# Performance work log

Measured on AMD Instinct MI355X. Metric: run time of the kernel, lower is better.

Reference implementation:

```python
import jax, jax.numpy as jnp
import numpy as np

# Static config (matches init_kwargs)
D_MODEL, H, L, P = 256, 8, 4, 4
HEAD_DIM = D_MODEL // H
SPATIAL = ((76, 114), (38, 57), (19, 29), (10, 15))  # (h, w) per level
NV = sum(h * w for h, w in SPATIAL)  # 11531
B, NQ = 2, NV


def setup_inputs() -> dict:
    key = jax.random.key(0)
    ks = jax.random.split(key, 12)
    inp = {
        "query": jax.random.normal(ks[0], (B, NQ, D_MODEL), jnp.float32),
        "reference_points": jax.random.uniform(ks[1], (B, NQ, L, 2), jnp.float32),
        "value": jax.random.normal(ks[2], (B, NV, D_MODEL), jnp.float32),
        # Linear params stored as [in, out] (i.e. torch weight transposed)
        "W_off": jax.random.normal(ks[3], (D_MODEL, H * L * P * 2), jnp.float32) * 0.02,
        "b_off": jax.random.normal(ks[4], (H * L * P * 2,), jnp.float32) * 0.5,
        "W_attn": jax.random.normal(ks[5], (D_MODEL, H * L * P), jnp.float32) * 0.02,
        "b_attn": jnp.zeros((H * L * P,), jnp.float32),
        "W_val": jax.random.normal(ks[6], (D_MODEL, D_MODEL), jnp.float32) * 0.05,
        "b_val": jnp.zeros((D_MODEL,), jnp.float32),
        "W_out": jax.random.normal(ks[7], (D_MODEL, D_MODEL), jnp.float32) * 0.05,
        "b_out": jnp.zeros((D_MODEL,), jnp.float32),
    }
    return inp


def _msda(query, reference_points, value, W_off, b_off, W_attn, b_attn,
          W_val, b_val, W_out, b_out):
    Bq, Nq, C = query.shape
    D = HEAD_DIM
    # value projection -> [B, H, Nv, D]
    v = (value @ W_val + b_val).reshape(Bq, -1, H, D).transpose(0, 2, 1, 3)
    # sampling locations: ref + offset / (w, h)  -> [B, Nq, H, L, P, 2] in [0,1] coords
    off = (query @ W_off + b_off).reshape(Bq, Nq, H, L, P, 2)
    wh = jnp.array([[w, h] for h, w in SPATIAL], dtype=query.dtype)  # [L, 2]
    loc = reference_points[:, :, None, :, None, :] + off / wh[None, None, None, :, None, :]
    # attention weights softmax over L*P  -> [B, H, Nq, L, P]
    attn = jax.nn.softmax((query @ W_attn + b_attn).reshape(Bq, Nq, H, L * P), axis=-1)
    attn = attn.reshape(Bq, Nq, H, L, P).transpose(0, 2, 1, 3, 4)
    starts = np.concatenate([[0], np.cumsum([h * w for h, w in SPATIAL])]).astype(int)
    out = jnp.zeros((Bq, H, Nq, D), query.dtype)
    for l, (lh, lw) in enumerate(SPATIAL):
        feat = v[:, :, starts[l]:starts[l + 1], :]  # [B, H, lh*lw, D]
        # grid_sample align_corners=False: pixel = loc * size - 0.5
        px = loc[:, :, :, l, :, 0].transpose(0, 2, 1, 3) * lw - 0.5  # [B, H, Nq, P]
        py = loc[:, :, :, l, :, 1].transpose(0, 2, 1, 3) * lh - 0.5
        x0 = jnp.floor(px)
        y0 = jnp.floor(py)
        samp = jnp.zeros(px.shape + (D,), query.dtype)
        for dx in (0, 1):
            for dy in (0, 1):
                xi = x0 + dx
                yi = y0 + dy
                w = (1.0 - jnp.abs(px - xi)) * (1.0 - jnp.abs(py - yi))
                valid = (xi >= 0) & (xi <= lw - 1) & (yi >= 0) & (yi <= lh - 1)
                idx = (jnp.clip(yi, 0, lh - 1) * lw + jnp.clip(xi, 0, lw - 1)).astype(jnp.int32)
                g = jnp.take_along_axis(feat, idx.reshape(Bq, H, -1)[..., None], axis=2)
                g = g.reshape(Bq, H, Nq, P, D)
                samp = samp + g * jnp.where(valid, w, 0.0)[..., None]
        out = out + jnp.einsum('bhnpd,bhnp->bhnd', samp, attn[:, :, :, l, :])
    out = out.transpose(0, 2, 1, 3).reshape(Bq, Nq, C)
    return out @ W_out + b_out


def reference(query, reference_points, value, W_off, b_off, W_attn, b_attn,
              W_val, b_val, W_out, b_out):
    return _msda(query, reference_points, value, W_off, b_off, W_attn, b_attn,
                 W_val, b_val, W_out, b_out)
```

## Files before the change

kernel.cpp:

```cpp
#include <hip/hip_runtime.h>
#include <cmath>

#define B_    2
#define NQ_   11531
#define NV_   11531
#define M_    (B_ * NQ_)
#define NCB_  2883

typedef unsigned short u16;
typedef unsigned int   u32;
typedef __attribute__((ext_vector_type(8))) short bf16x8;
typedef __attribute__((ext_vector_type(4))) float f32x4;

__device__ __forceinline__ u16 f2bf(float f) {
    union { float f; unsigned u; } v; v.f = f;
    unsigned r = v.u + 0x7FFFu + ((v.u >> 16) & 1u);
    return (u16)(r >> 16);
}
__device__ __forceinline__ float lo_bf(u32 u) {
    union { unsigned u; float f; } v; v.u = u << 16; return v.f;
}
__device__ __forceinline__ float hi_bf(u32 u) {
    union { unsigned u; float f; } v; v.u = u & 0xFFFF0000u; return v.f;
}

__device__ __forceinline__ int sort_key(const float* __restrict__ refp, int bq) {
    const int b = bq / NQ_;
    const float2 r = *(const float2*)&refp[(size_t)bq * 8];
    int qx = (int)(r.x * 32.f); qx = min(max(qx, 0), 31);
    int qy = (int)(r.y * 32.f); qy = min(max(qy, 0), 31);
    return b * 1024 + qy * 32 + qx;
}

__global__ __launch_bounds__(256) void transpose_hist_cast(
    const float* __restrict__ Wv, const float* __restrict__ Wo,
    const float* __restrict__ Wa, const float* __restrict__ Wu,
    const float* __restrict__ refp,
    const float* __restrict__ query, const float* __restrict__ value,
    u16* __restrict__ Tv, u16* __restrict__ Toa, u16* __restrict__ Tu,
    int* __restrict__ hist, u16* __restrict__ qbf, u16* __restrict__ vbf) {
    const int bid = blockIdx.x;
    const int tid = threadIdx.x;
    if (bid >= 347) {
        const int t8 = bid - 347;
        const bool isq = t8 < NCB_;
        const int cb = isq ? t8 : t8 - NCB_;
        const float* S = isq ? query : value;
        u16* D = isq ? qbf : vbf;
        const size_t TOT = (size_t)M_ * 256;
        const size_t e = ((size_t)cb * 256 + tid) * 8;
        if (e + 8 <= TOT) {
            const float4 a = *(const float4*)&S[e];
            const float4 b = *(const float4*)&S[e + 4];
            ushort4 lo, hi;
            lo.x = f2bf(a.x); lo.y = f2bf(a.y); lo.z = f2bf(a.z); lo.w = f2bf(a.w);
            hi.x = f2bf(b.x); hi.y = f2bf(b.y); hi.z = f2bf(b.z); hi.w = f2bf(b.w);
            *(ushort4*)&D[e] = lo;
            *(ushort4*)&D[e + 4] = hi;
        } else {
            for (size_t i = e; i < TOT; ++i) D[i] = f2bf(S[i]);
        }
        return;
    }
    if (bid >= 256) {
        const int bq = (bid - 256) * 256 + tid;
        if (bq < M_) atomicAdd(&hist[sort_key(refp, bq)], 1);
        return;
    }
    const int z = bid >> 6;
    const float* W; u16* T; int N; int rowoff = 0;
    if (z == 0)      { W = Wv; T = Tv;  N = 256; }
    else if (z == 1) { W = Wo; T = Toa; N = 256; }
    else if (z == 2) { W = Wa; T = Toa; N = 128; rowoff = 256; }
    else             { W = Wu; T = Tu;  N = 256; }
    const int rest = bid & 63;
    const int n0 = (rest & 7) * 32, k0 = (rest >> 3) * 32;
    if (n0 >= N) return;
    __shared__ float t[32][33];
    const int c = tid & 31, r0 = tid >> 5;
#pragma unroll
    for (int i = 0; i < 4; ++i)
        t[r0 + i * 8][c] = W[(size_t)(k0 + r0 + i * 8) * N + n0 + c];
    __syncthreads();
#pragma unroll
    for (int i = 0; i < 4; ++i)
        T[(size_t)(rowoff + n0 + r0 + i * 8) * 256 + k0 + c] = f2bf(t[c][r0 + i * 8]);
}

__device__ void scan_block(const int* __restrict__ hist, int* __restrict__ ofs,
                           int* part) {
    const int tid = threadIdx.x;
    const int base = tid * 8;
    int loc[8]; int s = 0;
#pragma unroll
    for (int i = 0; i < 8; ++i) { loc[i] = s; s += hist[base + i]; }
    part[tid] = s;
    __syncthreads();
    for (int d = 1; d < 256; d <<= 1) {
        const int v = part[tid];
        const int u = (tid >= d) ? part[tid - d] : 0;
        __syncthreads();
        part[tid] = v + u;
        __syncthreads();
    }
    const int off = (tid > 0) ? part[tid - 1] : 0;
#pragma unroll
    for (int i = 0; i < 8; ++i) ofs[base + i] = off + loc[i];
}

__global__ __launch_bounds__(256) void repack_scatter(
    const u16* __restrict__ ws_v, const float* __restrict__ refp,
    int* __restrict__ ofs, int* __restrict__ perm,
    u32* __restrict__ v3, int nsc) {
    const int bid = blockIdx.x;
    const int tid = threadIdx.x;
    if (bid < nsc) {
        const int bq = bid * 256 + tid;
        if (bq < M_) {
            const int pos = atomicAdd(&ofs[sort_key(refp, bq)], 1);
            perm[pos] = bq;
        }
        return;
    }
    const int g4 = (bid - nsc) * 256 + tid;
    if (g4 >= 8 * M_ * 8) return;
    const int h = g4 / (M_ * 8);
    const int rem = g4 - h * (M_ * 8);
    const int r = rem >> 3;
    const int c = (rem & 7) * 4;
    const ushort4 lo = *(const ushort4*)&ws_v[(size_t)r * 256 + h * 32 + c];
    ushort4 hi = make_ushort4(0, 0, 0, 0);
    if (r + 1 < M_) hi = *(const ushort4*)&ws_v[(size_t)(r + 1) * 256 + h * 32 + c];
    uint4 o;
    o.x = (u32)lo.x | ((u32)hi.x << 16);
    o.y = (u32)lo.y | ((u32)hi.y << 16);
    o.z = (u32)lo.z | ((u32)hi.z << 16);
    o.w = (u32)lo.w | ((u32)hi.w << 16);
    *(uint4*)&v3[((size_t)h * M_ + r) * 32 + c] = o;
}

template <int TN, int EPI>
__device__ __forceinline__ void gemm_body(const u16* __restrict__ A,
                                          const u16* __restrict__ WT,
                                          const float* __restrict__ bias,
                                          const float* __restrict__ bias2,
                                          void* __restrict__ Cv, int M,
                                          int bm, int bn,
                                          short* A_l, short* B_l) {
    constexpr int K = 256;
    const int tid = threadIdx.x;
    const int w = tid >> 6;
    const int lane = tid & 63;
    const int wr = (w >> 1) * 64;
    const int wc = (w & 1) * 64;
    const int lr = lane & 15;

    f32x4 acc[4][4] = {};

    for (int k0 = 0; k0 < K; k0 += 64) {
#pragma unroll
        for (int i = 0; i < 4; ++i) {
            const int vid = tid + i * 256;
            const int ar = vid >> 3;
            const int ak = (vid & 7) * 8;
            const int gr = bm + ar;
            uint4 hv = make_uint4(0u, 0u, 0u, 0u);
            if (gr < M) hv = *(const uint4*)&A[(size_t)gr * K + k0 + ak];
            *(uint4*)&A_l[ar * 72 + ak] = hv;
        }
#pragma unroll
        for (int i = 0; i < 4; ++i) {
            const int vid = tid + i * 256;
            const int nr = vid >> 3;
            const int kk = (vid & 7) * 8;
            const uint4 wv = *(const uint4*)&WT[(size_t)(bn + nr) * K + k0 + kk];
            *(uint4*)&B_l[nr * 72 + kk] = wv;
        }
        __syncthreads();
#pragma unroll
        for (int half = 0; half < 2; ++half) {
            const int kg = half * 32 + (lane >> 4) * 8;
            bf16x8 af[4], bfr[4];
#pragma unroll
            for (int m = 0; m < 4; ++m)
                af[m] = *(const bf16x8*)&A_l[(wr + m * 16 + lr) * 72 + kg];
#pragma unroll
            for (int n = 0; n < 4; ++n)
                bfr[n] = *(const bf16x8*)&B_l[(wc + n * 16 + lr) * 72 + kg];
#pragma unroll
            for (int m = 0; m < 4; ++m)
#pragma unroll
                for (int n = 0; n < 4; ++n)
                    acc[m][n] = __builtin_amdgcn_mfma_f32_16x16x32_bf16(af[m], bfr[n], acc[m][n], 0, 0, 0);
        }
        __syncthreads();
    }

#pragma unroll
    for (int n = 0; n < 4; ++n) {
        const int gcol = bn + wc + n * 16 + lr;
        const float bv = (TN == 384 && gcol >= 256) ? bias2[gcol - 256] : bias[gcol];
#pragma unroll
        for (int m = 0; m < 4; ++m) {
            const int rbase = bm + wr + m * 16 + (lane >> 4) * 4;
#pragma unroll
            for (int j = 0; j < 4; ++j) {
                const int grow = rbase + j;
                if (grow < M) {
                    const float o = acc[m][n][j] + bv;
                    if constexpr (EPI == 1) ((u16*)Cv)[(size_t)grow * TN + gcol] = f2bf(o);
                    else                    ((float*)Cv)[(size_t)grow * TN + gcol] = o;
                }
            }
        }
    }
}

__global__ __launch_bounds__(256, 4) void gemm_stage1(
    const u16* __restrict__ qbf, const u16* __restrict__ vbf,
    const u16* __restrict__ WT_val, const u16* __restrict__ WT_oa,
    const float* __restrict__ b_val, const float* __restrict__ b_off,
    const float* __restrict__ b_attn,
    const int* __restrict__ hist, int* __restrict__ ofs,
    u16* __restrict__ ws_v, float* __restrict__ ws_oa, int M, int gy) {
    __shared__ __align__(16) short A_l[128 * 72];
    __shared__ __align__(16) short B_l[128 * 72];
    int blk = blockIdx.x;
    if (blk == 5 * gy) {
        scan_block(hist, ofs, (int*)A_l);
    } else if (blk < 2 * gy) {
        gemm_body<256, 1>(vbf, WT_val, b_val, b_val, ws_v, M,
                          (blk >> 1) * 128, (blk & 1) * 128, A_l, B_l);
    } else {
        blk -= 2 * gy;
        gemm_body<384, 0>(qbf, WT_oa, b_off, b_attn, ws_oa, M,
                          (blk / 3) * 128, (blk % 3) * 128, A_l, B_l);
    }
}

__global__ __launch_bounds__(256, 4) void gemm_out(
    const u16* __restrict__ samp, const u16* __restrict__ WT_out,
    const float* __restrict__ b_out, float* __restrict__ out, int M) {
    __shared__ __align__(16) short A_l[128 * 72];
    __shared__ __align__(16) short B_l[128 * 72];
    const int blk = blockIdx.x;
    gemm_body<256, 0>(samp, WT_out, b_out, b_out, out, M,
                      (blk >> 1) * 128, (blk & 1) * 128, A_l, B_l);
}

__global__ __launch_bounds__(512, 4) void msda_sample_v10(
    const u32* __restrict__ v3,
    const float* __restrict__ oa,
    const float* __restrict__ refp,
    const int* __restrict__ perm,
    u16* __restrict__ samp) {
    __shared__ __align__(16) float4 s_w4[1088];
    __shared__ __align__(8)  int2   s_i2[1088];
    __shared__ int s_bq[8];
    const int tid = threadIdx.x;

    const int nwg = gridDim.x;
    const int qq = nwg >> 3, rr = nwg & 7;
    const int xcd = blockIdx.x & 7, pos = blockIdx.x >> 3;
    const int wg = (xcd < rr ? xcd * (qq + 1) : rr * (qq + 1) + (xcd - rr) * qq) + pos;
    const int bq0 = wg * 8;

    if (tid < 8) {
        const int q = bq0 + tid;
        s_bq[tid] = perm[q < M_ ? q : M_ - 1];
    }
    __syncthreads();

#pragma unroll
    for (int half = 0; half < 2; ++half) {
        const int s = tid + half * 512;
        const int qi = s >> 7;
        const int rem = s & 127;
        const int sampi = rem & 15;
        const int l = sampi >> 2;
        const int h = rem >> 4;
        const int bq = s_bq[qi];
        const int b = bq / NQ_;

        const float logit = oa[(size_t)bq * 384 + 256 + rem];
        float mx = logit;
#pragma unroll
        for (int t = 8; t >= 1; t >>= 1) mx = fmaxf(mx, __shfl_xor(mx, t, 16));
        const float e = __expf(logit - mx);
        float sm = e;
#pragma unroll
        for (int t = 8; t >= 1; t >>= 1) sm += __shfl_xor(sm, t, 16);
        const float aw = e / sm;

        const float2 off = *(const float2*)&oa[(size_t)bq * 384 + rem * 2];
        const float2 rxy = *(const float2*)&refp[(size_t)bq * 8 + l * 2];
        const int lw = (l == 0) ? 114 : (l == 1) ? 57 : (l == 2) ? 29 : 15;
        const int lh = (l == 0) ? 76 : (l == 1) ? 38 : (l == 2) ? 19 : 10;
        const int st = (l == 0) ? 0 : (l == 1) ? 8664 : (l == 2) ? 10830 : 11381;
        const int base = b * NV_ + st;

        const float px = rxy.x * (float)lw + off.x - 0.5f;
        const float py = rxy.y * (float)lh + off.y - 0.5f;
        const float x0f = floorf(px), y0f = floorf(py);
        const int x0 = (int)x0f, y0 = (int)y0f;
        const float fx = px - x0f, fy = py - y0f;

        float wxlo = 0.f, wxhi = 0.f;
        if (x0 >= 0 && x0 < lw)      wxlo = 1.f - fx;
        else if (x0 == -1)           wxlo = fx;
        if (x0 >= 0 && x0 + 1 < lw)  wxhi = fx;
        const int xs = min(max(x0, 0), lw - 1);

        const float wy0 = (y0 >= 0 && y0 < lh) ? (1.f - fy) : 0.f;
        const float wy1 = (y0 + 1 >= 0 && y0 + 1 < lh) ? fy : 0.f;
        const int ys0 = min(max(y0, 0), lh - 1);
        const int ys1 = min(max(y0 + 1, 0), lh - 1);

        const int hrow = h * M_;
        int2 iv;
        iv.x = (hrow + base + ys0 * lw + xs) << 7;
        iv.y = (hrow + base + ys1 * lw + xs) << 7;
        float4 wv;
        wv.x = aw * wxlo * wy0; wv.y = aw * wxhi * wy0;
        wv.z = aw * wxlo * wy1; wv.w = aw * wxhi * wy1;
        const int slot = (qi * 8 + h) * 17 + sampi;
        s_w4[slot] = wv;
        s_i2[slot] = iv;
    }
    __syncthreads();

    const int qi = tid >> 6;
    const int lane = tid & 63;
    const int h = lane >> 3;
    const int lcoff = (lane & 7) * 16;
    const int bq = s_bq[qi];
    const int sb = (qi * 8 + h) * 17;
    const char* vb = (const char*)v3;

    float acc0 = 0.f, acc1 = 0.f, acc2 = 0.f, acc3 = 0.f;
    float4 wc = s_w4[sb];
    int2 ic = s_i2[sb];
    uint4 A0 = *(const uint4*)(vb + (u32)(ic.x + lcoff));
    uint4 A1 = *(const uint4*)(vb + (u32)(ic.y + lcoff));

#pragma unroll 2
    for (int sp = 0; sp < 16; ++sp) {
        const int nxt = (sp + 1) & 15;
        const float4 wn = s_w4[sb + nxt];
        const int2 in_ = s_i2[sb + nxt];
        const uint4 B0 = *(const uint4*)(vb + (u32)(in_.x + lcoff));
        const uint4 B1 = *(const uint4*)(vb + (u32)(in_.y + lcoff));

        acc0 = fmaf(wc.x, lo_bf(A0.x), acc0); acc0 = fmaf(wc.y, hi_bf(A0.x), acc0);
        acc0 = fmaf(wc.z, lo_bf(A1.x), acc0); acc0 = fmaf(wc.w, hi_bf(A1.x), acc0);
        acc1 = fmaf(wc.x, lo_bf(A0.y), acc1); acc1 = fmaf(wc.y, hi_bf(A0.y), acc1);
        acc1 = fmaf(wc.z, lo_bf(A1.y), acc1); acc1 = fmaf(wc.w, hi_bf(A1.y), acc1);
        acc2 = fmaf(wc.x, lo_bf(A0.z), acc2); acc2 = fmaf(wc.y, hi_bf(A0.z), acc2);
        acc2 = fmaf(wc.z, lo_bf(A1.z), acc2); acc2 = fmaf(wc.w, hi_bf(A1.z), acc2);
        acc3 = fmaf(wc.x, lo_bf(A0.w), acc3); acc3 = fmaf(wc.y, hi_bf(A0.w), acc3);
        acc3 = fmaf(wc.z, lo_bf(A1.w), acc3); acc3 = fmaf(wc.w, hi_bf(A1.w), acc3);

        wc = wn; A0 = B0; A1 = B1;
    }
    if (bq0 + qi < M_) {
        ushort4 o;
        o.x = f2bf(acc0); o.y = f2bf(acc1); o.z = f2bf(acc2); o.w = f2bf(acc3);
        *(ushort4*)&samp[(size_t)bq * 256 + (h * 32 + (lane & 7) * 4)] = o;
    }
}

extern "C" void kernel_launch(void* const* d_in, const int* in_sizes, int n_in,
                              void* d_out, int out_size, void* d_ws, size_t ws_size,
                              hipStream_t stream) {
    const float* query  = (const float*)d_in[0];
    const float* refp   = (const float*)d_in[1];
    const float* value  = (const float*)d_in[2];
    const float* W_off  = (const float*)d_in[3];
    const float* b_off  = (const float*)d_in[4];
    const float* W_attn = (const float*)d_in[5];
    const float* b_attn = (const float*)d_in[6];
    const float* W_val  = (const float*)d_in[7];
    const float* b_val  = (const float*)d_in[8];
    const float* W_out  = (const float*)d_in[9];
    const float* b_out  = (const float*)d_in[10];
    float* out = (float*)d_out;

    const int M = M_;
    u16*   ws_v    = (u16*)d_ws;
    u16*   ws_samp = ws_v;
    u32*   ws_v3   = (u32*)(ws_v + (size_t)M * 256);
    u16*   vbf     = (u16*)ws_v3;
    float* ws_oa   = (float*)(ws_v3 + (size_t)8 * M * 32);
    u16*   qbf     = (u16*)(ws_oa + (size_t)M * 384);
    u16*   WT_val  = qbf + (size_t)M * 256;
    u16*   WT_oa   = WT_val + 256 * 256;
    u16*   WT_out  = WT_oa + 384 * 256;
    int*   hist    = (int*)(WT_out + 256 * 256);
    int*   ofs     = hist + 2048;
    int*   perm    = ofs + 2048;

    const int gy = (M + 127) / 128;
    const int gq = (M + 255) / 256;
    const int grep = (8 * M * 8 + 255) / 256;

    hipMemsetAsync(hist, 0, 2048 * sizeof(int), stream);
    transpose_hist_cast<<<dim3(347 + 2 * NCB_), 256, 0, stream>>>(
        W_val, W_off, W_attn, W_out, refp, query, value,
        WT_val, WT_oa, WT_out, hist, qbf, vbf);
    gemm_stage1<<<dim3(5 * gy + 1), 256, 0, stream>>>(qbf, vbf, WT_val, WT_oa,
                                                      b_val, b_off, b_attn,
                                                      hist, ofs, ws_v, ws_oa, M, gy);
    repack_scatter<<<dim3(gq + grep), 256, 0, stream>>>(ws_v, refp, ofs, perm,
                                                        ws_v3, gq);
    msda_sample_v10<<<dim3((M + 7) / 8), 512, 0, stream>>>(ws_v3, ws_oa, refp, perm, ws_samp);
    gemm_out<<<dim3(2 * gy), 256, 0, stream>>>(ws_samp, WT_out, b_out, out, M);
}
```

Measured before the change: 113.7 us.

## Shrink GEMM tiles to 64x64 with K=32 steps and pack sampling FMAs

The shared GEMM body moves from 128x128 tiles with K steps of 64 to 64x64 tiles with K steps of 32. This quadruples the number of blocks and raises the occupancy hint to 8, so more workgroups cover the ~23k-row problems with less LDS per block. In exchange each tile does less reuse and hits more barriers per K. Separately, the sampling kernel's bilinear accumulation uses two-wide float vectors so the compiler can emit packed FMA (v_pk_fma), with the two partial sums added at the end. That changes the floating-point summation order slightly.

```diff
diff --git a/kernel.cpp b/kernel.cpp
--- a/kernel.cpp
+++ b/kernel.cpp
@@ -11,17 +11,17 @@
 typedef unsigned int   u32;
 typedef __attribute__((ext_vector_type(8))) short bf16x8;
 typedef __attribute__((ext_vector_type(4))) float f32x4;
+typedef __attribute__((ext_vector_type(2))) float f32x2;
 
 __device__ __forceinline__ u16 f2bf(float f) {
     union { float f; unsigned u; } v; v.f = f;
     unsigned r = v.u + 0x7FFFu + ((v.u >> 16) & 1u);
     return (u16)(r >> 16);
 }
-__device__ __forceinline__ float lo_bf(u32 u) {
-    union { unsigned u; float f; } v; v.u = u << 16; return v.f;
-}
-__device__ __forceinline__ float hi_bf(u32 u) {
-    union { unsigned u; float f; } v; v.u = u & 0xFFFF0000u; return v.f;
+__device__ __forceinline__ f32x2 unpk(u32 u) {
+    union { unsigned u; float f; } lo, hi;
+    lo.u = u << 16; hi.u = u & 0xFFFF0000u;
+    f32x2 r; r.x = lo.f; r.y = hi.f; return r;
 }
 
 __device__ __forceinline__ int sort_key(const float* __restrict__ refp, int bq) {
@@ -151,57 +151,50 @@
     const int tid = threadIdx.x;
     const int w = tid >> 6;
     const int lane = tid & 63;
-    const int wr = (w >> 1) * 64;
-    const int wc = (w & 1) * 64;
+    const int wr = (w >> 1) * 32;
+    const int wc = (w & 1) * 32;
     const int lr = lane & 15;
-
-    f32x4 acc[4][4] = {};
-
-    for (int k0 = 0; k0 < K; k0 += 64) {
-#pragma unroll
-        for (int i = 0; i < 4; ++i) {
-            const int vid = tid + i * 256;
-            const int ar = vid >> 3;
-            const int ak = (vid & 7) * 8;
+    const int kg = (lane >> 4) * 8;
+
+    f32x4 acc[2][2] = {};
+
+    for (int k0 = 0; k0 < K; k0 += 32) {
+        {
+            const int ar = tid >> 2;
+            const int ak = (tid & 3) * 8;
             const int gr = bm + ar;
             uint4 hv = make_uint4(0u, 0u, 0u, 0u);
             if (gr < M) hv = *(const uint4*)&A[(size_t)gr * K + k0 + ak];
-            *(uint4*)&A_l[ar * 72 + ak] = hv;
+            *(uint4*)&A_l[ar * 40 + ak] = hv;
         }
-#pragma unroll
-        for (int i = 0; i < 4; ++i) {
-            const int vid = tid + i * 256;
-            const int nr = vid >> 3;
-            const int kk = (vid & 7) * 8;
+        {
+            const int nr = tid >> 2;
+            const int kk = (tid & 3) * 8;
             const uint4 wv = *(const uint4*)&WT[(size_t)(bn + nr) * K + k0 + kk];
-            *(uint4*)&B_l[nr * 72 + kk] = wv;
+            *(uint4*)&B_l[nr * 40 + kk] = wv;
         }
         __syncthreads();
-#pragma unroll
-        for (int half = 0; half < 2; ++half) {
-            const int kg = half * 32 + (lane >> 4) * 8;
-            bf16x8 af[4], bfr[4];
-#pragma unroll
-            for (int m = 0; m < 4; ++m)
-                af[m] = *(const bf16x8*)&A_l[(wr + m * 16 + lr) * 72 + kg];
-#pragma unroll
-            for (int n = 0; n < 4; ++n)
-                bfr[n] = *(const bf16x8*)&B_l[(wc + n * 16 + lr) * 72 + kg];
-#pragma unroll
-            for (int m = 0; m < 4; ++m)
-#pragma unroll
-                for (int n = 0; n < 4; ++n)
-                    acc[m][n] = __builtin_amdgcn_mfma_f32_16x16x32_bf16(af[m], bfr[n], acc[m][n], 0, 0, 0);
-        }
+        bf16x8 af[2], bfr[2];
+#pragma unroll
+        for (int m = 0; m < 2; ++m)
+            af[m] = *(const bf16x8*)&A_l[(wr + m * 16 + lr) * 40 + kg];
+#pragma unroll
+        for (int n = 0; n < 2; ++n)
+            bfr[n] = *(const bf16x8*)&B_l[(wc + n * 16 + lr) * 40 + kg];
+#pragma unroll
+        for (int m = 0; m < 2; ++m)
+#pragma unroll
+            for (int n = 0; n < 2; ++n)
+                acc[m][n] = __builtin_amdgcn_mfma_f32_16x16x32_bf16(af[m], bfr[n], acc[m][n], 0, 0, 0);
         __syncthreads();
     }
 
 #pragma unroll
-    for (int n = 0; n < 4; ++n) {
+    for (int n = 0; n < 2; ++n) {
         const int gcol = bn + wc + n * 16 + lr;
         const float bv = (TN == 384 && gcol >= 256) ? bias2[gcol - 256] : bias[gcol];
 #pragma unroll
-        for (int m = 0; m < 4; ++m) {
+        for (int m = 0; m < 2; ++m) {
             const int rbase = bm + wr + m * 16 + (lane >> 4) * 4;
 #pragma unroll
             for (int j = 0; j < 4; ++j) {
@@ -216,39 +209,40 @@
     }
 }
 
-__global__ __launch_bounds__(256, 4) void gemm_stage1(
+__global__ __launch_bounds__(256, 8) void gemm_stage1(
     const u16* __restrict__ qbf, const u16* __restrict__ vbf,
     const u16* __restrict__ WT_val, const u16* __restrict__ WT_oa,
     const float* __restrict__ b_val, const float* __restrict__ b_off,
     const float* __restrict__ b_attn,
     const int* __restrict__ hist, int* __restrict__ ofs,
-    u16* __restrict__ ws_v, float* __restrict__ ws_oa, int M, int gy) {
-    __shared__ __align__(16) short A_l[128 * 72];
-    __shared__ __align__(16) short B_l[128 * 72];
+    u16* __restrict__ ws_v, float* __restrict__ ws_oa, int M, int gy64) {
+    __shared__ __align__(16) short A_l[64 * 40];
+    __shared__ __align__(16) short B_l[64 * 40];
+    __shared__ int part[256];
     int blk = blockIdx.x;
-    if (blk == 5 * gy) {
-        scan_block(hist, ofs, (int*)A_l);
-    } else if (blk < 2 * gy) {
+    if (blk == 10 * gy64) {
+        scan_block(hist, ofs, part);
+    } else if (blk < 4 * gy64) {
         gemm_body<256, 1>(vbf, WT_val, b_val, b_val, ws_v, M,
-                          (blk >> 1) * 128, (blk & 1) * 128, A_l, B_l);
+                          (blk >> 2) * 64, (blk & 3) * 64, A_l, B_l);
     } else {
-        blk -= 2 * gy;
+        blk -= 4 * gy64;
         gemm_body<384, 0>(qbf, WT_oa, b_off, b_attn, ws_oa, M,
-                          (blk / 3) * 128, (blk % 3) * 128, A_l, B_l);
-    }
-}
-
-__global__ __launch_bounds__(256, 4) void gemm_out(
+                          (blk / 6) * 64, (blk % 6) * 64, A_l, B_l);
+    }
+}
+
+__global__ __launch_bounds__(256, 8) void gemm_out(
     const u16* __restrict__ samp, const u16* __restrict__ WT_out,
     const float* __restrict__ b_out, float* __restrict__ out, int M) {
-    __shared__ __align__(16) short A_l[128 * 72];
-    __shared__ __align__(16) short B_l[128 * 72];
+    __shared__ __align__(16) short A_l[64 * 40];
+    __shared__ __align__(16) short B_l[64 * 40];
     const int blk = blockIdx.x;
     gemm_body<256, 0>(samp, WT_out, b_out, b_out, out, M,
-                      (blk >> 1) * 128, (blk & 1) * 128, A_l, B_l);
-}
-
-__global__ __launch_bounds__(512, 4) void msda_sample_v10(
+                      (blk >> 2) * 64, (blk & 3) * 64, A_l, B_l);
+}
+
+__global__ __launch_bounds__(512, 4) void msda_sample_v11(
     const u32* __restrict__ v3,
     const float* __restrict__ oa,
     const float* __restrict__ refp,
@@ -337,8 +331,8 @@
     const int sb = (qi * 8 + h) * 17;
     const char* vb = (const char*)v3;
 
-    float acc0 = 0.f, acc1 = 0.f, acc2 = 0.f, acc3 = 0.f;
-    float4 wc = s_w4[sb];
+    f32x2 acc0 = {0.f, 0.f}, acc1 = {0.f, 0.f}, acc2 = {0.f, 0.f}, acc3 = {0.f, 0.f};
+    float4 wcur = s_w4[sb];
     int2 ic = s_i2[sb];
     uint4 A0 = *(const uint4*)(vb + (u32)(ic.x + lcoff));
     uint4 A1 = *(const uint4*)(vb + (u32)(ic.y + lcoff));
@@ -351,20 +345,19 @@
         const uint4 B0 = *(const uint4*)(vb + (u32)(in_.x + lcoff));
         const uint4 B1 = *(const uint4*)(vb + (u32)(in_.y + lcoff));
 
-        acc0 = fmaf(wc.x, lo_bf(A0.x), acc0); acc0 = fmaf(wc.y, hi_bf(A0.x), acc0);
-        acc0 = fmaf(wc.z, lo_bf(A1.x), acc0); acc0 = fmaf(wc.w, hi_bf(A1.x), acc0);
-        acc1 = fmaf(wc.x, lo_bf(A0.y), acc1); acc1 = fmaf(wc.y, hi_bf(A0.y), acc1);
-        acc1 = fmaf(wc.z, lo_bf(A1.y), acc1); acc1 = fmaf(wc.w, hi_bf(A1.y), acc1);
-        acc2 = fmaf(wc.x, lo_bf(A0.z), acc2); acc2 = fmaf(wc.y, hi_bf(A0.z), acc2);
-        acc2 = fmaf(wc.z, lo_bf(A1.z), acc2); acc2 = fmaf(wc.w, hi_bf(A1.z), acc2);
-        acc3 = fmaf(wc.x, lo_bf(A0.w), acc3); acc3 = fmaf(wc.y, hi_bf(A0.w), acc3);
-        acc3 = fmaf(wc.z, lo_bf(A1.w), acc3); acc3 = fmaf(wc.w, hi_bf(A1.w), acc3);
-
-        wc = wn; A0 = B0; A1 = B1;
+        f32x2 w01; w01.x = wcur.x; w01.y = wcur.y;
+        f32x2 w23; w23.x = wcur.z; w23.y = wcur.w;
+        acc0 += unpk(A0.x) * w01; acc0 += unpk(A1.x) * w23;
+        acc1 += unpk(A0.y) * w01; acc1 += unpk(A1.y) * w23;
+        acc2 += unpk(A0.z) * w01; acc2 += unpk(A1.z) * w23;
+        acc3 += unpk(A0.w) * w01; acc3 += unpk(A1.w) * w23;
+
+        wcur = wn; A0 = B0; A1 = B1;
     }
     if (bq0 + qi < M_) {
         ushort4 o;
-        o.x = f2bf(acc0); o.y = f2bf(acc1); o.z = f2bf(acc2); o.w = f2bf(acc3);
+        o.x = f2bf(acc0.x + acc0.y); o.y = f2bf(acc1.x + acc1.y);
+        o.z = f2bf(acc2.x + acc2.y); o.w = f2bf(acc3.x + acc3.y);
         *(ushort4*)&samp[(size_t)bq * 256 + (h * 32 + (lane & 7) * 4)] = o;
     }
 }
@@ -399,7 +392,7 @@
     int*   ofs     = hist + 2048;
     int*   perm    = ofs + 2048;
 
-    const int gy = (M + 127) / 128;
+    const int gy64 = (M + 63) / 64;
     const int gq = (M + 255) / 256;
     const int grep = (8 * M * 8 + 255) / 256;
 
@@ -407,11 +400,11 @@
     transpose_hist_cast<<<dim3(347 + 2 * NCB_), 256, 0, stream>>>(
         W_val, W_off, W_attn, W_out, refp, query, value,
         WT_val, WT_oa, WT_out, hist, qbf, vbf);
-    gemm_stage1<<<dim3(5 * gy + 1), 256, 0, stream>>>(qbf, vbf, WT_val, WT_oa,
-                                                      b_val, b_off, b_attn,
-                                                      hist, ofs, ws_v, ws_oa, M, gy);
+    gemm_stage1<<<dim3(10 * gy64 + 1), 256, 0, stream>>>(qbf, vbf, WT_val, WT_oa,
+                                                         b_val, b_off, b_attn,
+                                                         hist, ofs, ws_v, ws_oa, M, gy64);
     repack_scatter<<<dim3(gq + grep), 256, 0, stream>>>(ws_v, refp, ofs, perm,
                                                         ws_v3, gq);
-    msda_sample_v10<<<dim3((M + 7) / 8), 512, 0, stream>>>(ws_v3, ws_oa, refp, perm, ws_samp);
-    gemm_out<<<dim3(2 * gy), 256, 0, stream>>>(ws_samp, WT_out, b_out, out, M);
-}
+    msda_sample_v11<<<dim3((M + 7) / 8), 512, 0, stream>>>(ws_v3, ws_oa, refp, perm, ws_samp);
+    gemm_out<<<dim3(4 * gy64), 256, 0, stream>>>(ws_samp, WT_out, b_out, out, M);
+}
```

Measured after the change: 115.6 us. No clear change (+1.7%).

## Store offset/attention logits as fp16 and use packed float2 FMAs in sampler

Applied to the files above, without the earlier changes.

The offset/attention GEMM epilogue now writes fp16 instead of fp32, halving the bytes written by stage 1 and read by the sampling kernel. The sampler decodes these halves. Its inner accumulation is restructured into two-wide vector multiply-adds so the compiler can emit packed FP32 instructions, with a final horizontal add per accumulator. This reduces memory traffic and ALU instruction count, at the cost of some precision in the sampling offsets (fp16 around 114-pixel coordinates) and a changed summation order.

```diff
diff --git a/kernel.cpp b/kernel.cpp
--- a/kernel.cpp
+++ b/kernel.cpp
@@ -11,17 +11,23 @@
 typedef unsigned int   u32;
 typedef __attribute__((ext_vector_type(8))) short bf16x8;
 typedef __attribute__((ext_vector_type(4))) float f32x4;
+typedef __attribute__((ext_vector_type(2))) float f32x2;
 
 __device__ __forceinline__ u16 f2bf(float f) {
     union { float f; unsigned u; } v; v.f = f;
     unsigned r = v.u + 0x7FFFu + ((v.u >> 16) & 1u);
     return (u16)(r >> 16);
 }
-__device__ __forceinline__ float lo_bf(u32 u) {
-    union { unsigned u; float f; } v; v.u = u << 16; return v.f;
-}
-__device__ __forceinline__ float hi_bf(u32 u) {
-    union { unsigned u; float f; } v; v.u = u & 0xFFFF0000u; return v.f;
+__device__ __forceinline__ u16 f2h(float f) {
+    union { _Float16 h; u16 u; } v; v.h = (_Float16)f; return v.u;
+}
+__device__ __forceinline__ float h2f(u16 u) {
+    union { u16 u; _Float16 h; } v; v.u = u; return (float)v.h;
+}
+__device__ __forceinline__ f32x2 unpk(u32 u) {
+    union { unsigned u; float f; } lo, hi;
+    lo.u = u << 16; hi.u = u & 0xFFFF0000u;
+    f32x2 r; r.x = lo.f; r.y = hi.f; return r;
 }
 
 __device__ __forceinline__ int sort_key(const float* __restrict__ refp, int bq) {
@@ -208,8 +214,9 @@
                 const int grow = rbase + j;
                 if (grow < M) {
                     const float o = acc[m][n][j] + bv;
-                    if constexpr (EPI == 1) ((u16*)Cv)[(size_t)grow * TN + gcol] = f2bf(o);
-                    else                    ((float*)Cv)[(size_t)grow * TN + gcol] = o;
+                    if constexpr (EPI == 1)      ((u16*)Cv)[(size_t)grow * TN + gcol] = f2bf(o);
+                    else if constexpr (EPI == 2) ((u16*)Cv)[(size_t)grow * TN + gcol] = f2h(o);
+                    else                         ((float*)Cv)[(size_t)grow * TN + gcol] = o;
                 }
             }
         }
@@ -222,7 +229,7 @@
     const float* __restrict__ b_val, const float* __restrict__ b_off,
     const float* __restrict__ b_attn,
     const int* __restrict__ hist, int* __restrict__ ofs,
-    u16* __restrict__ ws_v, float* __restrict__ ws_oa, int M, int gy) {
+    u16* __restrict__ ws_v, u16* __restrict__ ws_oa, int M, int gy) {
     __shared__ __align__(16) short A_l[128 * 72];
     __shared__ __align__(16) short B_l[128 * 72];
     int blk = blockIdx.x;
@@ -233,7 +240,7 @@
                           (blk >> 1) * 128, (blk & 1) * 128, A_l, B_l);
     } else {
         blk -= 2 * gy;
-        gemm_body<384, 0>(qbf, WT_oa, b_off, b_attn, ws_oa, M,
+        gemm_body<384, 2>(qbf, WT_oa, b_off, b_attn, ws_oa, M,
                           (blk / 3) * 128, (blk % 3) * 128, A_l, B_l);
     }
 }
@@ -248,9 +255,9 @@
                       (blk >> 1) * 128, (blk & 1) * 128, A_l, B_l);
 }
 
-__global__ __launch_bounds__(512, 4) void msda_sample_v10(
+__global__ __launch_bounds__(512, 4) void msda_sample_v12(
     const u32* __restrict__ v3,
-    const float* __restrict__ oa,
+    const u16* __restrict__ oa,
     const float* __restrict__ refp,
     const int* __restrict__ perm,
     u16* __restrict__ samp) {
@@ -281,8 +288,9 @@
         const int h = rem >> 4;
         const int bq = s_bq[qi];
         const int b = bq / NQ_;
-
-        const float logit = oa[(size_t)bq * 384 + 256 + rem];
+        const u16* oar = oa + (size_t)bq * 384;
+
+        const float logit = h2f(oar[256 + rem]);
         float mx = logit;
 #pragma unroll
         for (int t = 8; t >= 1; t >>= 1) mx = fmaxf(mx, __shfl_xor(mx, t, 16));
@@ -292,15 +300,17 @@
         for (int t = 8; t >= 1; t >>= 1) sm += __shfl_xor(sm, t, 16);
         const float aw = e / sm;
 
-        const float2 off = *(const float2*)&oa[(size_t)bq * 384 + rem * 2];
+        const u32 op = *(const u32*)&oar[rem * 2];
+        const float offx = h2f((u16)op);
+        const float offy = h2f((u16)(op >> 16));
         const float2 rxy = *(const float2*)&refp[(size_t)bq * 8 + l * 2];
         const int lw = (l == 0) ? 114 : (l == 1) ? 57 : (l == 2) ? 29 : 15;
         const int lh = (l == 0) ? 76 : (l == 1) ? 38 : (l == 2) ? 19 : 10;
         const int st = (l == 0) ? 0 : (l == 1) ? 8664 : (l == 2) ? 10830 : 11381;
         const int base = b * NV_ + st;
 
-        const float px = rxy.x * (float)lw + off.x - 0.5f;
-        const float py = rxy.y * (float)lh + off.y - 0.5f;
+        const float px = rxy.x * (float)lw + offx - 0.5f;
+        const float py = rxy.y * (float)lh + offy - 0.5f;
         const float x0f = floorf(px), y0f = floorf(py);
         const int x0 = (int)x0f, y0 = (int)y0f;
         const float fx = px - x0f, fy = py - y0f;
@@ -337,8 +347,8 @@
     const int sb = (qi * 8 + h) * 17;
     const char* vb = (const char*)v3;
 
-    float acc0 = 0.f, acc1 = 0.f, acc2 = 0.f, acc3 = 0.f;
-    float4 wc = s_w4[sb];
+    f32x2 acc0 = {0.f, 0.f}, acc1 = {0.f, 0.f}, acc2 = {0.f, 0.f}, acc3 = {0.f, 0.f};
+    float4 wcur = s_w4[sb];
     int2 ic = s_i2[sb];
     uint4 A0 = *(const uint4*)(vb + (u32)(ic.x + lcoff));
     uint4 A1 = *(const uint4*)(vb + (u32)(ic.y + lcoff));
@@ -351,20 +361,19 @@
         const uint4 B0 = *(const uint4*)(vb + (u32)(in_.x + lcoff));
         const uint4 B1 = *(const uint4*)(vb + (u32)(in_.y + lcoff));
 
-        acc0 = fmaf(wc.x, lo_bf(A0.x), acc0); acc0 = fmaf(wc.y, hi_bf(A0.x), acc0);
-        acc0 = fmaf(wc.z, lo_bf(A1.x), acc0); acc0 = fmaf(wc.w, hi_bf(A1.x), acc0);
-        acc1 = fmaf(wc.x, lo_bf(A0.y), acc1); acc1 = fmaf(wc.y, hi_bf(A0.y), acc1);
-        acc1 = fmaf(wc.z, lo_bf(A1.y), acc1); acc1 = fmaf(wc.w, hi_bf(A1.y), acc1);
-        acc2 = fmaf(wc.x, lo_bf(A0.z), acc2); acc2 = fmaf(wc.y, hi_bf(A0.z), acc2);
-        acc2 = fmaf(wc.z, lo_bf(A1.z), acc2); acc2 = fmaf(wc.w, hi_bf(A1.z), acc2);
-        acc3 = fmaf(wc.x, lo_bf(A0.w), acc3); acc3 = fmaf(wc.y, hi_bf(A0.w), acc3);
-        acc3 = fmaf(wc.z, lo_bf(A1.w), acc3); acc3 = fmaf(wc.w, hi_bf(A1.w), acc3);
-
-        wc = wn; A0 = B0; A1 = B1;
+        f32x2 w01; w01.x = wcur.x; w01.y = wcur.y;
+        f32x2 w23; w23.x = wcur.z; w23.y = wcur.w;
+        acc0 += unpk(A0.x) * w01; acc0 += unpk(A1.x) * w23;
+        acc1 += unpk(A0.y) * w01; acc1 += unpk(A1.y) * w23;
+        acc2 += unpk(A0.z) * w01; acc2 += unpk(A1.z) * w23;
+        acc3 += unpk(A0.w) * w01; acc3 += unpk(A1.w) * w23;
+
+        wcur = wn; A0 = B0; A1 = B1;
     }
     if (bq0 + qi < M_) {
         ushort4 o;
-        o.x = f2bf(acc0); o.y = f2bf(acc1); o.z = f2bf(acc2); o.w = f2bf(acc3);
+        o.x = f2bf(acc0.x + acc0.y); o.y = f2bf(acc1.x + acc1.y);
+        o.z = f2bf(acc2.x + acc2.y); o.w = f2bf(acc3.x + acc3.y);
         *(ushort4*)&samp[(size_t)bq * 256 + (h * 32 + (lane & 7) * 4)] = o;
     }
 }
@@ -390,8 +399,8 @@
     u16*   ws_samp = ws_v;
     u32*   ws_v3   = (u32*)(ws_v + (size_t)M * 256);
     u16*   vbf     = (u16*)ws_v3;
-    float* ws_oa   = (float*)(ws_v3 + (size_t)8 * M * 32);
-    u16*   qbf     = (u16*)(ws_oa + (size_t)M * 384);
+    u16*   ws_oa   = (u16*)(ws_v3 + (size_t)8 * M * 32);
+    u16*   qbf     = ws_oa + (size_t)M * 384;
     u16*   WT_val  = qbf + (size_t)M * 256;
     u16*   WT_oa   = WT_val + 256 * 256;
     u16*   WT_out  = WT_oa + 384 * 256;
@@ -412,6 +421,6 @@
                                                       hist, ofs, ws_v, ws_oa, M, gy);
     repack_scatter<<<dim3(gq + grep), 256, 0, stream>>>(ws_v, refp, ofs, perm,
                                                         ws_v3, gq);
-    msda_sample_v10<<<dim3((M + 7) / 8), 512, 0, stream>>>(ws_v3, ws_oa, refp, perm, ws_samp);
+    msda_sample_v12<<<dim3((M + 7) / 8), 512, 0, stream>>>(ws_v3, ws_oa, refp, perm, ws_samp);
     gemm_out<<<dim3(2 * gy), 256, 0, stream>>>(ws_samp, WT_out, b_out, out, M);
 }
```

After: 113.0 us. No clear change (-0.6%).
